# Optimization experiments

Measured on AMD Instinct MI355X. Metric: run time of the kernel, lower is better.

Reference implementation:

```python
import jax, jax.numpy as jnp
import numpy as np

FG_FRACTION = 0.5
BATCHSIZE = 256
NUM_IMAGES = 1
NUM_CLASSES = 21
FG_THRESH = 0.5
BG_THRESH_HI = 0.5
BG_THRESH_LO = 0.1
ROIS_PER_IMAGE = BATCHSIZE // NUM_IMAGES                      # 256
FG_ROIS_PER_IMAGE = int(round(FG_FRACTION * ROIS_PER_IMAGE))  # 128
BG_ROIS_PER_IMAGE = ROIS_PER_IMAGE - FG_ROIS_PER_IMAGE        # 128


def _make_boxes(key, n, img=1000.0, max_wh=200.0):
    k1, k2 = jax.random.split(key)
    xy = jax.random.uniform(k1, (n, 2), dtype=jnp.float32) * (img - max_wh)
    wh = jax.random.uniform(k2, (n, 2), dtype=jnp.float32) * max_wh + 1.0
    return jnp.concatenate([xy, xy + wh], axis=1)  # valid [x1,y1,x2,y2]


def setup_inputs() -> dict:
    key = jax.random.key(0)
    k1, k2, k3 = jax.random.split(key, 3)
    N, G = 250000, 128
    rois = _make_boxes(k1, N)
    all_rois = jnp.concatenate([jnp.zeros((N, 1), jnp.float32), rois], axis=1)  # [N,5], col0 = image idx
    gt_boxes = _make_boxes(k2, G)                                               # [G,4]
    gt_labels = jax.random.randint(k3, (G,), 1, NUM_CLASSES).astype(jnp.int32)  # fg classes 1..20
    return {"all_rois": all_rois, "gt_boxes": gt_boxes, "gt_labels": gt_labels}


def _iou(a, b):
    area_a = (a[:, 2] - a[:, 0] + 1.0) * (a[:, 3] - a[:, 1] + 1.0)
    area_b = (b[:, 2] - b[:, 0] + 1.0) * (b[:, 3] - b[:, 1] + 1.0)
    ix1 = jnp.maximum(a[:, None, 0], b[None, :, 0])
    iy1 = jnp.maximum(a[:, None, 1], b[None, :, 1])
    ix2 = jnp.minimum(a[:, None, 2], b[None, :, 2])
    iy2 = jnp.minimum(a[:, None, 3], b[None, :, 3])
    iw = jnp.clip(ix2 - ix1 + 1.0, 0.0)
    ih = jnp.clip(iy2 - iy1 + 1.0, 0.0)
    inter = iw * ih
    return inter / (area_a[:, None] + area_b[None, :] - inter)


def _bbox_transform(ex, gt):
    ew = ex[:, 2] - ex[:, 0] + 1.0
    eh = ex[:, 3] - ex[:, 1] + 1.0
    ecx = ex[:, 0] + 0.5 * ew
    ecy = ex[:, 1] + 0.5 * eh
    gw = gt[:, 2] - gt[:, 0] + 1.0
    gh = gt[:, 3] - gt[:, 1] + 1.0
    gcx = gt[:, 0] + 0.5 * gw
    gcy = gt[:, 1] + 0.5 * gh
    return jnp.stack([(gcx - ecx) / ew, (gcy - ecy) / eh,
                      jnp.log(gw / ew), jnp.log(gh / eh)], axis=1)


def _proposal_target(all_rois, gt_boxes, gt_labels):
    G = gt_boxes.shape[0]
    # append gt boxes (with image-index 0 column) to the proposal set
    gt_rois = jnp.concatenate([jnp.zeros((G, 1), all_rois.dtype), gt_boxes], axis=1)
    all_rois = jnp.concatenate([all_rois, gt_rois], axis=0)          # [N+G, 5]

    overlaps = _iou(all_rois[:, 1:5], gt_boxes)                       # [N+G, G] -- dominant memory traffic
    gt_assignment = jnp.argmax(overlaps, axis=1)                      # [N+G]
    max_ov = jnp.max(overlaps, axis=1)                                # [N+G]
    labels_all = gt_labels[gt_assignment]                             # [N+G]

    fg_mask = max_ov >= FG_THRESH
    bg_mask = (max_ov < BG_THRESH_HI) & (max_ov >= BG_THRESH_LO)

    # random fg/bg sampling: top-k over random keys restricted to each mask
    u = jax.random.uniform(jax.random.key(42), (all_rois.shape[0],), dtype=jnp.float32)
    fg_idx = jax.lax.top_k(jnp.where(fg_mask, u, -1.0), FG_ROIS_PER_IMAGE)[1]
    bg_idx = jax.lax.top_k(jnp.where(bg_mask, u, -1.0), BG_ROIS_PER_IMAGE)[1]
    keep = jnp.concatenate([fg_idx, bg_idx])                          # [256]

    valid_fg = fg_mask[fg_idx]  # if fewer fg than requested, pad slots get label 0
    labels = jnp.concatenate([jnp.where(valid_fg, labels_all[fg_idx], 0),
                              jnp.zeros((BG_ROIS_PER_IMAGE,), labels_all.dtype)])

    rois = all_rois[keep]                                             # [256, 5]
    targets = _bbox_transform(rois[:, 1:5], gt_boxes[gt_assignment[keep]])  # [256, 4]

    # scatter targets into class-specific columns [256, 4*num_classes]
    onehot = jax.nn.one_hot(labels, NUM_CLASSES, dtype=targets.dtype)
    bbox_targets = (onehot[:, :, None] * targets[:, None, :]).reshape(ROIS_PER_IMAGE, 4 * NUM_CLASSES)
    bbox_targets = bbox_targets * (labels > 0)[:, None].astype(targets.dtype)
    return rois, labels, bbox_targets


def reference(all_rois, gt_boxes, gt_labels):
    return _proposal_target(all_rois, gt_boxes, gt_labels)
```

## Files before the change

### kernel.cpp

```cpp
#include <hip/hip_runtime.h>
#include <stdint.h>

#define GMAX 128
#define TK 128
#define NBINS 4096
#define CAND_MAX 4096
#define NUM_CLASSES 21

typedef float f32x4u __attribute__((ext_vector_type(4), aligned(4)));

__device__ __forceinline__ void threefry2x32(uint32_t k0, uint32_t k1,
                                             uint32_t& x0, uint32_t& x1) {
  uint32_t ks0 = k0, ks1 = k1, ks2 = k0 ^ k1 ^ 0x1BD11BDAu;
  x0 += ks0; x1 += ks1;
#define TF_ROUND(r) { x0 += x1; x1 = (x1 << (r)) | (x1 >> (32 - (r))); x1 ^= x0; }
  TF_ROUND(13) TF_ROUND(15) TF_ROUND(26) TF_ROUND(6)
  x0 += ks1; x1 += ks2 + 1u;
  TF_ROUND(17) TF_ROUND(29) TF_ROUND(16) TF_ROUND(24)
  x0 += ks2; x1 += ks0 + 2u;
  TF_ROUND(13) TF_ROUND(15) TF_ROUND(26) TF_ROUND(6)
  x0 += ks0; x1 += ks1 + 3u;
  TF_ROUND(17) TF_ROUND(29) TF_ROUND(16) TF_ROUND(24)
  x0 += ks1; x1 += ks2 + 4u;
  TF_ROUND(13) TF_ROUND(15) TF_ROUND(26) TF_ROUND(6)
  x0 += ks2; x1 += ks0 + 5u;
#undef TF_ROUND
}

__global__ void __launch_bounds__(512)
score_kernel(const float* __restrict__ all_rois,
             const float* __restrict__ gt_boxes,
             uint32_t* __restrict__ score,
             uint32_t* __restrict__ hist,
             int* __restrict__ meta,
             int N, int M, int G) {
  __shared__ uint64_t lds_key[256];
  __shared__ float sga[GMAX];
  const int t = threadIdx.x;
  const int lane = t & 63;
  const int wave = t >> 6;
  const int wq = wave & 3;
  const int half = __builtin_amdgcn_readfirstlane(wave >> 2);
  const int i = blockIdx.x * 256 + wq * 64 + lane;
  const bool active = (i < M);

  const float4* __restrict__ gt4 = reinterpret_cast<const float4*>(gt_boxes);
  if (t < GMAX) {
    float4 b = gt4[t];
    sga[t] = __fmul_rn(__fadd_rn(__fsub_rn(b.z, b.x), 1.0f),
                       __fadd_rn(__fsub_rn(b.w, b.y), 1.0f));
  }

  float bx1 = 0.0f, by1 = 0.0f, bx2 = 0.0f, by2 = 0.0f;
  if (active) {
    if (i < N) {
      f32x4u v = *reinterpret_cast<const f32x4u*>(all_rois + (size_t)i * 5 + 1);
      bx1 = v.x; by1 = v.y; bx2 = v.z; by2 = v.w;
    } else {
      float4 b = gt4[i - N];
      bx1 = b.x; by1 = b.y; bx2 = b.z; by2 = b.w;
    }
  }
  const float area = __fmul_rn(__fadd_rn(__fsub_rn(bx2, bx1), 1.0f),
                               __fadd_rn(__fsub_rn(by2, by1), 1.0f));
  __syncthreads();

  float best = -1.0f;
  int bi = 0;
  const int g0 = half * 64;
#pragma unroll 8
  for (int g = 0; g < 64; ++g) {
    const float4 gb = gt4[g0 + g];
    const float ga = sga[g0 + g];
    float ix1 = fmaxf(bx1, gb.x);
    float iy1 = fmaxf(by1, gb.y);
    float ix2 = fminf(bx2, gb.z);
    float iy2 = fminf(by2, gb.w);
    float iw = fmaxf(__fadd_rn(__fsub_rn(ix2, ix1), 1.0f), 0.0f);
    float ih = fmaxf(__fadd_rn(__fsub_rn(iy2, iy1), 1.0f), 0.0f);
    float inter = __fmul_rn(iw, ih);
    float uni = __fsub_rn(__fadd_rn(area, ga), inter);
    float ov = __fdiv_rn(inter, uni);
    if (ov > best) { best = ov; bi = g0 + g; }
  }

  const uint64_t mykey = ((uint64_t)__float_as_uint(best) << 32) |
                         (uint64_t)(uint32_t)(127 - bi);
  if (half == 1) lds_key[wq * 64 + lane] = mykey;
  __syncthreads();

  if (half == 0) {
    uint64_t kk = lds_key[wq * 64 + lane];
    if (mykey > kk) kk = mykey;
    best = __uint_as_float((uint32_t)(kk >> 32));
    bi = 127 - (int)(kk & 127ull);

    if (active) {
      uint32_t cx0 = 0u, cx1 = (uint32_t)i;
      threefry2x32(0u, 42u, cx0, cx1);
      uint32_t ubits = (cx0 ^ cx1) >> 9;
      uint32_t fg = (best >= 0.5f) ? 1u : 0u;
      uint32_t bg = (!fg && best >= 0.1f) ? 1u : 0u;
      score[i] = (ubits << 9) | ((uint32_t)bi << 2) | (fg << 1) | bg;
      if (fg)      atomicAdd(&hist[ubits >> 11], 1u);
      else if (bg) atomicAdd(&hist[NBINS + (ubits >> 11)], 1u);
    }
  }

  asm volatile("s_waitcnt vmcnt(0)" ::: "memory");
  __syncthreads();
  __shared__ unsigned s_prev;
  if (t == 0) s_prev = atomicAdd((unsigned int*)&meta[2], 1u);
  __syncthreads();
  if (s_prev != gridDim.x - 1) return;

  __shared__ uint64_t gs[512];
  __shared__ int s_jstar[2];
  const int b0 = 8 * t;
  uint64_t acc = 0;
  for (int k = 0; k < 8; ++k) {
    uint32_t hf = __hip_atomic_load(&hist[b0 + k], __ATOMIC_RELAXED,
                                    __HIP_MEMORY_SCOPE_AGENT);
    uint32_t hb = __hip_atomic_load(&hist[NBINS + b0 + k], __ATOMIC_RELAXED,
                                    __HIP_MEMORY_SCOPE_AGENT);
    acc += ((uint64_t)hf << 32) | (uint64_t)hb;
  }
  gs[t] = acc;
  if (t < 2) s_jstar[t] = -1;
  __syncthreads();
  for (int d = 1; d < 512; d <<= 1) {
    uint64_t add = (t + d < 512) ? gs[t + d] : 0ull;
    __syncthreads();
    gs[t] += add;
    __syncthreads();
  }
  uint32_t vfg = (uint32_t)(gs[t] >> 32);
  uint32_t vbg = (uint32_t)gs[t];
  uint32_t nfg = (t < 511) ? (uint32_t)(gs[t + 1] >> 32) : 0u;
  uint32_t nbg = (t < 511) ? (uint32_t)gs[t + 1] : 0u;
  if (vfg >= (uint32_t)TK && (t == 511 || nfg < (uint32_t)TK)) s_jstar[0] = t;
  if (vbg >= (uint32_t)TK && (t == 511 || nbg < (uint32_t)TK)) s_jstar[1] = t;
  __syncthreads();
  if (t == 0) {
    for (int m = 0; m < 2; ++m) {
      int j = s_jstar[m], B = -1;
      if (j >= 0) {
        uint32_t base = 0;
        if (j < 511)
          base = (m == 0) ? (uint32_t)(gs[j + 1] >> 32) : (uint32_t)gs[j + 1];
        B = 8 * j;
        for (int b = 8 * j + 7; b >= 8 * j; --b) {
          base += __hip_atomic_load(&hist[m * NBINS + b], __ATOMIC_RELAXED,
                                    __HIP_MEMORY_SCOPE_AGENT);
          if (base >= (uint32_t)TK) { B = b; break; }
        }
      }
      meta[4 + m] = B;
    }
  }
}

__global__ void __launch_bounds__(256)
compact_kernel(const uint32_t* __restrict__ score, int M,
               int* __restrict__ meta,
               uint64_t* __restrict__ cand) {
  const int bth[2] = {meta[4], meta[5]};
  const int base = (blockIdx.x * 256 + threadIdx.x) * 4;
  if (base >= M) return;
  uint32_t ss[4];
  int lim;
  if (base + 3 < M) {
    uint4 s4 = *reinterpret_cast<const uint4*>(score + base);
    ss[0] = s4.x; ss[1] = s4.y; ss[2] = s4.z; ss[3] = s4.w;
    lim = 4;
  } else {
    lim = M - base;
    for (int k = 0; k < lim; ++k) ss[k] = score[base + k];
  }
  for (int k = 0; k < lim; ++k) {
    uint32_t s = ss[k];
    uint32_t mb = s & 3u;
    if (!mb) continue;
    int m = (mb & 2u) ? 0 : 1;
    int B = bth[m];
    if (B >= 0 && (int)(s >> 20) < B) continue;
    int p = atomicAdd(&meta[m], 1);
    if (p < CAND_MAX)
      cand[(size_t)m * CAND_MAX + p] =
          (((uint64_t)((s >> 9) + 1u)) << 32) | (uint64_t)(~(uint32_t)(base + k));
  }
}

__global__ void __launch_bounds__(1024)
final_kernel(const float* __restrict__ all_rois,
             const float* __restrict__ gt_boxes,
             const int* __restrict__ gt_labels,
             const uint32_t* __restrict__ score,
             const uint64_t* __restrict__ cand_g,
             const int* __restrict__ meta,
             float* __restrict__ out, int N, int M) {
  __shared__ uint64_t cand[CAND_MAX];
  __shared__ int keep[2 * TK];
  __shared__ int fgvalid[TK];
  __shared__ float s_tx[2 * TK], s_ty[2 * TK], s_tw[2 * TK], s_th[2 * TK];
  __shared__ int s_label[2 * TK];
  const int t = threadIdx.x;

  for (int m = 0; m < 2; ++m) {
    int cnt = meta[m]; if (cnt > CAND_MAX) cnt = CAND_MAX;
    for (int p = t; p < cnt; p += 1024)
      cand[p] = cand_g[(size_t)m * CAND_MAX + p];
    __syncthreads();
    for (int p = t; p < cnt; p += 1024) {
      uint64_t key = cand[p];
      int r = 0;
      for (int j = 0; j < cnt; ++j) r += (cand[j] > key) ? 1 : 0;
      if (r < TK) {
        keep[m * TK + r] = (int)(~(uint32_t)(key & 0xFFFFFFFFull));
        if (m == 0) fgvalid[r] = 1;
      }
    }
    __syncthreads();
    if (cnt < TK && t == 0) {
      int fill = cnt;
      uint32_t mask_bit = (m == 0) ? 2u : 1u;
      for (int i2 = 0; i2 < M && fill < TK; ++i2)
        if (!(score[i2] & mask_bit)) {
          keep[m * TK + fill] = i2;
          if (m == 0) fgvalid[fill] = 0;
          fill++;
        }
    }
    __syncthreads();
  }

  const int R = 2 * TK;
  float* rois_out   = out;
  float* labels_out = out + (size_t)R * 5;
  float* bt_out     = out + (size_t)R * 5 + R;

  if (t < R) {
    const int i = keep[t];
    float rimg, rx1, ry1, rx2, ry2;
    if (i < N) {
      rimg = all_rois[(size_t)i * 5 + 0];
      rx1  = all_rois[(size_t)i * 5 + 1];
      ry1  = all_rois[(size_t)i * 5 + 2];
      rx2  = all_rois[(size_t)i * 5 + 3];
      ry2  = all_rois[(size_t)i * 5 + 4];
    } else {
      int g = i - N;
      rimg = 0.0f;
      rx1 = gt_boxes[g * 4 + 0]; ry1 = gt_boxes[g * 4 + 1];
      rx2 = gt_boxes[g * 4 + 2]; ry2 = gt_boxes[g * 4 + 3];
    }
    rois_out[t * 5 + 0] = rimg;
    rois_out[t * 5 + 1] = rx1;
    rois_out[t * 5 + 2] = ry1;
    rois_out[t * 5 + 3] = rx2;
    rois_out[t * 5 + 4] = ry2;

    const int ga = (int)((score[i] >> 2) & 127u);
    int label = (t < TK && fgvalid[t]) ? gt_labels[ga] : 0;
    labels_out[t] = (float)label;
    s_label[t] = label;

    float gx1 = gt_boxes[ga * 4 + 0], gy1 = gt_boxes[ga * 4 + 1];
    float gx2 = gt_boxes[ga * 4 + 2], gy2 = gt_boxes[ga * 4 + 3];
    float ew = rx2 - rx1 + 1.0f, eh = ry2 - ry1 + 1.0f;
    float ecx = rx1 + 0.5f * ew, ecy = ry1 + 0.5f * eh;
    float gw = gx2 - gx1 + 1.0f, gh = gy2 - gy1 + 1.0f;
    float gcx = gx1 + 0.5f * gw, gcy = gy1 + 0.5f * gh;
    s_tx[t] = (gcx - ecx) / ew;
    s_ty[t] = (gcy - ecy) / eh;
    s_tw[t] = logf(gw / ew);
    s_th[t] = logf(gh / eh);
  }
  __syncthreads();

  const int TOT = R * 4 * NUM_CLASSES;
  for (int idx = t; idx < TOT; idx += 1024) {
    int r = idx / (4 * NUM_CLASSES);
    int c = idx - r * (4 * NUM_CLASSES);
    int lab = s_label[r];
    float v = 0.0f;
    if (lab > 0 && (c >> 2) == lab) {
      int cc = c & 3;
      v = (cc == 0) ? s_tx[r] : (cc == 1) ? s_ty[r] : (cc == 2) ? s_tw[r] : s_th[r];
    }
    bt_out[idx] = v;
  }
}

extern "C" void kernel_launch(void* const* d_in, const int* in_sizes, int n_in,
                              void* d_out, int out_size, void* d_ws, size_t ws_size,
                              hipStream_t stream) {
  const float* all_rois = (const float*)d_in[0];
  const float* gt_boxes = (const float*)d_in[1];
  const int*   gt_labels = (const int*)d_in[2];
  const int N = in_sizes[0] / 5;
  const int G = in_sizes[2];
  const int M = N + G;

  char* ws = (char*)d_ws;
  int* meta = (int*)ws;
  uint32_t* hist = (uint32_t*)(ws + 256);
  size_t off = 256 + (size_t)2 * NBINS * 4;
  uint32_t* score = (uint32_t*)(ws + off);
  off += (((size_t)M * 4) + 255) & ~(size_t)255;
  uint64_t* cand = (uint64_t*)(ws + off);
  float* out = (float*)d_out;

  hipMemsetAsync(ws, 0, 256 + (size_t)2 * NBINS * 4, stream);
  const int nblocks = (M + 255) / 256;
  score_kernel<<<nblocks, 512, 0, stream>>>(all_rois, gt_boxes, score,
                                            hist, meta, N, M, G);
  const int nb4 = ((M + 3) / 4 + 255) / 256;
  compact_kernel<<<nb4, 256, 0, stream>>>(score, M, meta, cand);
  final_kernel<<<1, 1024, 0, stream>>>(all_rois, gt_boxes, gt_labels, score,
                                       cand, meta, out, N, M);
}
```

Before: 109.9 us.

## Fuse score, compaction and final selection into one kernel via last-block tail

Merges the three kernels into a single launch: the last block to finish scoring computes the histogram thresholds, compacts candidates into shared memory using LDS atomics, ranks them and writes the outputs. This removes two kernel launches and the global candidate buffer round trip. In exchange, compaction of all ~250k scores now runs serially on one 512-thread block. The larger static LDS footprint may also lower occupancy in the scoring phase, and the shared candidate capacity shrinks to 2048 per class.

Measured after the change: 192.0 us. 1.75x slower.

```diff
diff --git a/kernel.cpp b/kernel.cpp
--- a/kernel.cpp
+++ b/kernel.cpp
@@ -4,7 +4,7 @@
 #define GMAX 128
 #define TK 128
 #define NBINS 4096
-#define CAND_MAX 4096
+#define CLDS 2048
 #define NUM_CLASSES 21
 
 typedef float f32x4u __attribute__((ext_vector_type(4), aligned(4)));
@@ -28,14 +28,31 @@
 }
 
 __global__ void __launch_bounds__(512)
-score_kernel(const float* __restrict__ all_rois,
+fused_kernel(const float* __restrict__ all_rois,
              const float* __restrict__ gt_boxes,
+             const int* __restrict__ gt_labels,
              uint32_t* __restrict__ score,
              uint32_t* __restrict__ hist,
              int* __restrict__ meta,
-             int N, int M, int G) {
-  __shared__ uint64_t lds_key[256];
-  __shared__ float sga[GMAX];
+             float* __restrict__ out,
+             int N, int M) {
+  __shared__ __align__(16) char smem[39488];
+  uint64_t* lds_key = (uint64_t*)smem;
+  float*    sga     = (float*)(smem + 2048);
+  uint64_t* gs      = (uint64_t*)smem;
+  uint64_t* cand    = (uint64_t*)smem;
+  int*      s_jstar = (int*)(smem + 32768);
+  int*      s_bth   = (int*)(smem + 32776);
+  int*      s_cnt   = (int*)(smem + 32784);
+  unsigned* s_prevp = (unsigned*)(smem + 32792);
+  int*      keep    = (int*)(smem + 32800);
+  int*      fgvalid = (int*)(smem + 33824);
+  int*      s_label = (int*)(smem + 34336);
+  float*    s_tx    = (float*)(smem + 35360);
+  float*    s_ty    = (float*)(smem + 36384);
+  float*    s_tw    = (float*)(smem + 37408);
+  float*    s_th    = (float*)(smem + 38432);
+
   const int t = threadIdx.x;
   const int lane = t & 63;
   const int wave = t >> 6;
@@ -50,7 +67,6 @@
     sga[t] = __fmul_rn(__fadd_rn(__fsub_rn(b.z, b.x), 1.0f),
                        __fadd_rn(__fsub_rn(b.w, b.y), 1.0f));
   }
-
   float bx1 = 0.0f, by1 = 0.0f, bx2 = 0.0f, by2 = 0.0f;
   if (active) {
     if (i < N) {
@@ -94,7 +110,6 @@
     if (mykey > kk) kk = mykey;
     best = __uint_as_float((uint32_t)(kk >> 32));
     bi = 127 - (int)(kk & 127ull);
-
     if (active) {
       uint32_t cx0 = 0u, cx1 = (uint32_t)i;
       threefry2x32(0u, 42u, cx0, cx1);
@@ -109,112 +124,94 @@
 
   asm volatile("s_waitcnt vmcnt(0)" ::: "memory");
   __syncthreads();
-  __shared__ unsigned s_prev;
-  if (t == 0) s_prev = atomicAdd((unsigned int*)&meta[2], 1u);
-  __syncthreads();
-  if (s_prev != gridDim.x - 1) return;
-
-  __shared__ uint64_t gs[512];
-  __shared__ int s_jstar[2];
-  const int b0 = 8 * t;
-  uint64_t acc = 0;
-  for (int k = 0; k < 8; ++k) {
-    uint32_t hf = __hip_atomic_load(&hist[b0 + k], __ATOMIC_RELAXED,
-                                    __HIP_MEMORY_SCOPE_AGENT);
-    uint32_t hb = __hip_atomic_load(&hist[NBINS + b0 + k], __ATOMIC_RELAXED,
-                                    __HIP_MEMORY_SCOPE_AGENT);
-    acc += ((uint64_t)hf << 32) | (uint64_t)hb;
-  }
-  gs[t] = acc;
-  if (t < 2) s_jstar[t] = -1;
-  __syncthreads();
-  for (int d = 1; d < 512; d <<= 1) {
-    uint64_t add = (t + d < 512) ? gs[t + d] : 0ull;
-    __syncthreads();
-    gs[t] += add;
-    __syncthreads();
-  }
-  uint32_t vfg = (uint32_t)(gs[t] >> 32);
-  uint32_t vbg = (uint32_t)gs[t];
-  uint32_t nfg = (t < 511) ? (uint32_t)(gs[t + 1] >> 32) : 0u;
-  uint32_t nbg = (t < 511) ? (uint32_t)gs[t + 1] : 0u;
-  if (vfg >= (uint32_t)TK && (t == 511 || nfg < (uint32_t)TK)) s_jstar[0] = t;
-  if (vbg >= (uint32_t)TK && (t == 511 || nbg < (uint32_t)TK)) s_jstar[1] = t;
-  __syncthreads();
-  if (t == 0) {
-    for (int m = 0; m < 2; ++m) {
-      int j = s_jstar[m], B = -1;
-      if (j >= 0) {
-        uint32_t base = 0;
-        if (j < 511)
-          base = (m == 0) ? (uint32_t)(gs[j + 1] >> 32) : (uint32_t)gs[j + 1];
-        B = 8 * j;
-        for (int b = 8 * j + 7; b >= 8 * j; --b) {
-          base += __hip_atomic_load(&hist[m * NBINS + b], __ATOMIC_RELAXED,
-                                    __HIP_MEMORY_SCOPE_AGENT);
-          if (base >= (uint32_t)TK) { B = b; break; }
+  if (t == 0)
+    *s_prevp = atomicAdd((unsigned int*)&meta[2], 1u);
+  __syncthreads();
+  if (*s_prevp != gridDim.x - 1) return;
+  __syncthreads();
+
+  {
+    const int b0 = 8 * t;
+    uint64_t acc = 0;
+    for (int k = 0; k < 8; ++k) {
+      uint32_t hf = __hip_atomic_load(&hist[b0 + k], __ATOMIC_RELAXED,
+                                      __HIP_MEMORY_SCOPE_AGENT);
+      uint32_t hb = __hip_atomic_load(&hist[NBINS + b0 + k], __ATOMIC_RELAXED,
+                                      __HIP_MEMORY_SCOPE_AGENT);
+      acc += ((uint64_t)hf << 32) | (uint64_t)hb;
+    }
+    gs[t] = acc;
+    if (t < 2) s_jstar[t] = -1;
+    __syncthreads();
+    for (int d = 1; d < 512; d <<= 1) {
+      uint64_t add = (t + d < 512) ? gs[t + d] : 0ull;
+      __syncthreads();
+      gs[t] += add;
+      __syncthreads();
+    }
+    uint32_t vfg = (uint32_t)(gs[t] >> 32);
+    uint32_t vbg = (uint32_t)gs[t];
+    uint32_t nfg = (t < 511) ? (uint32_t)(gs[t + 1] >> 32) : 0u;
+    uint32_t nbg = (t < 511) ? (uint32_t)gs[t + 1] : 0u;
+    if (vfg >= (uint32_t)TK && (t == 511 || nfg < (uint32_t)TK)) s_jstar[0] = t;
+    if (vbg >= (uint32_t)TK && (t == 511 || nbg < (uint32_t)TK)) s_jstar[1] = t;
+    __syncthreads();
+    if (t == 0) {
+      for (int m = 0; m < 2; ++m) {
+        int j = s_jstar[m], B = -1;
+        if (j >= 0) {
+          uint32_t base = 0;
+          if (j < 511)
+            base = (m == 0) ? (uint32_t)(gs[j + 1] >> 32) : (uint32_t)gs[j + 1];
+          B = 8 * j;
+          for (int b = 8 * j + 7; b >= 8 * j; --b) {
+            base += __hip_atomic_load(&hist[m * NBINS + b], __ATOMIC_RELAXED,
+                                      __HIP_MEMORY_SCOPE_AGENT);
+            if (base >= (uint32_t)TK) { B = b; break; }
+          }
         }
+        s_bth[m] = B;
       }
-      meta[4 + m] = B;
-    }
-  }
-}
-
-__global__ void __launch_bounds__(256)
-compact_kernel(const uint32_t* __restrict__ score, int M,
-               int* __restrict__ meta,
-               uint64_t* __restrict__ cand) {
-  const int bth[2] = {meta[4], meta[5]};
-  const int base = (blockIdx.x * 256 + threadIdx.x) * 4;
-  if (base >= M) return;
-  uint32_t ss[4];
-  int lim;
-  if (base + 3 < M) {
-    uint4 s4 = *reinterpret_cast<const uint4*>(score + base);
-    ss[0] = s4.x; ss[1] = s4.y; ss[2] = s4.z; ss[3] = s4.w;
-    lim = 4;
-  } else {
-    lim = M - base;
-    for (int k = 0; k < lim; ++k) ss[k] = score[base + k];
-  }
-  for (int k = 0; k < lim; ++k) {
-    uint32_t s = ss[k];
-    uint32_t mb = s & 3u;
-    if (!mb) continue;
-    int m = (mb & 2u) ? 0 : 1;
-    int B = bth[m];
-    if (B >= 0 && (int)(s >> 20) < B) continue;
-    int p = atomicAdd(&meta[m], 1);
-    if (p < CAND_MAX)
-      cand[(size_t)m * CAND_MAX + p] =
-          (((uint64_t)((s >> 9) + 1u)) << 32) | (uint64_t)(~(uint32_t)(base + k));
-  }
-}
-
-__global__ void __launch_bounds__(1024)
-final_kernel(const float* __restrict__ all_rois,
-             const float* __restrict__ gt_boxes,
-             const int* __restrict__ gt_labels,
-             const uint32_t* __restrict__ score,
-             const uint64_t* __restrict__ cand_g,
-             const int* __restrict__ meta,
-             float* __restrict__ out, int N, int M) {
-  __shared__ uint64_t cand[CAND_MAX];
-  __shared__ int keep[2 * TK];
-  __shared__ int fgvalid[TK];
-  __shared__ float s_tx[2 * TK], s_ty[2 * TK], s_tw[2 * TK], s_th[2 * TK];
-  __shared__ int s_label[2 * TK];
-  const int t = threadIdx.x;
+    }
+    if (t < 2) s_cnt[t] = 0;
+    __syncthreads();
+  }
+
+  {
+    const int bth0 = s_bth[0], bth1 = s_bth[1];
+    for (int base = t * 4; base < M; base += 512 * 4) {
+      uint32_t ss[4];
+      int lim;
+      if (base + 3 < M) {
+        uint4 s4 = *reinterpret_cast<const uint4*>(score + base);
+        ss[0] = s4.x; ss[1] = s4.y; ss[2] = s4.z; ss[3] = s4.w;
+        lim = 4;
+      } else {
+        lim = M - base;
+        for (int k = 0; k < lim; ++k) ss[k] = score[base + k];
+      }
+      for (int k = 0; k < lim; ++k) {
+        uint32_t s = ss[k];
+        uint32_t mb = s & 3u;
+        if (!mb) continue;
+        int m = (mb & 2u) ? 0 : 1;
+        int B = (m == 0) ? bth0 : bth1;
+        if (B >= 0 && (int)(s >> 20) < B) continue;
+        int p = atomicAdd(&s_cnt[m], 1);
+        if (p < CLDS)
+          cand[m * CLDS + p] = (((uint64_t)((s >> 9) + 1u)) << 32) |
+                               (uint64_t)(~(uint32_t)(base + k));
+      }
+    }
+    __syncthreads();
+  }
 
   for (int m = 0; m < 2; ++m) {
-    int cnt = meta[m]; if (cnt > CAND_MAX) cnt = CAND_MAX;
-    for (int p = t; p < cnt; p += 1024)
-      cand[p] = cand_g[(size_t)m * CAND_MAX + p];
-    __syncthreads();
-    for (int p = t; p < cnt; p += 1024) {
-      uint64_t key = cand[p];
+    int cnt = s_cnt[m]; if (cnt > CLDS) cnt = CLDS;
+    for (int p = t; p < cnt; p += 512) {
+      uint64_t key = cand[m * CLDS + p];
       int r = 0;
-      for (int j = 0; j < cnt; ++j) r += (cand[j] > key) ? 1 : 0;
+      for (int j = 0; j < cnt; ++j) r += (cand[m * CLDS + j] > key) ? 1 : 0;
       if (r < TK) {
         keep[m * TK + r] = (int)(~(uint32_t)(key & 0xFFFFFFFFull));
         if (m == 0) fgvalid[r] = 1;
@@ -240,16 +237,16 @@
   float* bt_out     = out + (size_t)R * 5 + R;
 
   if (t < R) {
-    const int i = keep[t];
+    const int ii = keep[t];
     float rimg, rx1, ry1, rx2, ry2;
-    if (i < N) {
-      rimg = all_rois[(size_t)i * 5 + 0];
-      rx1  = all_rois[(size_t)i * 5 + 1];
-      ry1  = all_rois[(size_t)i * 5 + 2];
-      rx2  = all_rois[(size_t)i * 5 + 3];
-      ry2  = all_rois[(size_t)i * 5 + 4];
+    if (ii < N) {
+      rimg = all_rois[(size_t)ii * 5 + 0];
+      rx1  = all_rois[(size_t)ii * 5 + 1];
+      ry1  = all_rois[(size_t)ii * 5 + 2];
+      rx2  = all_rois[(size_t)ii * 5 + 3];
+      ry2  = all_rois[(size_t)ii * 5 + 4];
     } else {
-      int g = i - N;
+      int g = ii - N;
       rimg = 0.0f;
       rx1 = gt_boxes[g * 4 + 0]; ry1 = gt_boxes[g * 4 + 1];
       rx2 = gt_boxes[g * 4 + 2]; ry2 = gt_boxes[g * 4 + 3];
@@ -260,13 +257,13 @@
     rois_out[t * 5 + 3] = rx2;
     rois_out[t * 5 + 4] = ry2;
 
-    const int ga = (int)((score[i] >> 2) & 127u);
-    int label = (t < TK && fgvalid[t]) ? gt_labels[ga] : 0;
+    const int ga2 = (int)((score[ii] >> 2) & 127u);
+    int label = (t < TK && fgvalid[t]) ? gt_labels[ga2] : 0;
     labels_out[t] = (float)label;
     s_label[t] = label;
 
-    float gx1 = gt_boxes[ga * 4 + 0], gy1 = gt_boxes[ga * 4 + 1];
-    float gx2 = gt_boxes[ga * 4 + 2], gy2 = gt_boxes[ga * 4 + 3];
+    float gx1 = gt_boxes[ga2 * 4 + 0], gy1 = gt_boxes[ga2 * 4 + 1];
+    float gx2 = gt_boxes[ga2 * 4 + 2], gy2 = gt_boxes[ga2 * 4 + 3];
     float ew = rx2 - rx1 + 1.0f, eh = ry2 - ry1 + 1.0f;
     float ecx = rx1 + 0.5f * ew, ecy = ry1 + 0.5f * eh;
     float gw = gx2 - gx1 + 1.0f, gh = gy2 - gy1 + 1.0f;
@@ -279,14 +276,15 @@
   __syncthreads();
 
   const int TOT = R * 4 * NUM_CLASSES;
-  for (int idx = t; idx < TOT; idx += 1024) {
+  for (int idx = t; idx < TOT; idx += 512) {
     int r = idx / (4 * NUM_CLASSES);
     int c = idx - r * (4 * NUM_CLASSES);
     int lab = s_label[r];
     float v = 0.0f;
     if (lab > 0 && (c >> 2) == lab) {
       int cc = c & 3;
-      v = (cc == 0) ? s_tx[r] : (cc == 1) ? s_ty[r] : (cc == 2) ? s_tw[r] : s_th[r];
+      v = (cc == 0) ? s_tx[r] : (cc == 1) ? s_ty[r]
+                              : (cc == 2) ? s_tw[r] : s_th[r];
     }
     bt_out[idx] = v;
   }
@@ -301,22 +299,16 @@
   const int N = in_sizes[0] / 5;
   const int G = in_sizes[2];
   const int M = N + G;
+  (void)G;
 
   char* ws = (char*)d_ws;
   int* meta = (int*)ws;
   uint32_t* hist = (uint32_t*)(ws + 256);
-  size_t off = 256 + (size_t)2 * NBINS * 4;
-  uint32_t* score = (uint32_t*)(ws + off);
-  off += (((size_t)M * 4) + 255) & ~(size_t)255;
-  uint64_t* cand = (uint64_t*)(ws + off);
+  uint32_t* score = (uint32_t*)(ws + 256 + (size_t)2 * NBINS * 4);
   float* out = (float*)d_out;
 
   hipMemsetAsync(ws, 0, 256 + (size_t)2 * NBINS * 4, stream);
   const int nblocks = (M + 255) / 256;
-  score_kernel<<<nblocks, 512, 0, stream>>>(all_rois, gt_boxes, score,
-                                            hist, meta, N, M, G);
-  const int nb4 = ((M + 3) / 4 + 255) / 256;
-  compact_kernel<<<nb4, 256, 0, stream>>>(score, M, meta, cand);
-  final_kernel<<<1, 1024, 0, stream>>>(all_rois, gt_boxes, gt_labels, score,
-                                       cand, meta, out, N, M);
+  fused_kernel<<<nblocks, 512, 0, stream>>>(all_rois, gt_boxes, gt_labels,
+                                            score, hist, meta, out, N, M);
 }
```
